# Kernel tuning notes

Measured on AMD Instinct MI355X. Metric: run time of the kernel, lower is better.

The kernel has to match this reference:

```python
import jax, jax.numpy as jnp
import numpy as np


def _hippo_scale_params(N, L):
    """Replicates HiPPOScale.__init__ for discretization='bilinear' (pure numpy)."""
    q = np.arange(N, dtype=np.float64)
    col, row = np.meshgrid(q, q)
    r = 2 * q + 1
    M = -(np.where(row >= col, r, 0) - np.diag(q))
    T = np.sqrt(np.diag(2 * q + 1))
    A = T @ M @ np.linalg.inv(T)          # (N, N)
    B = np.diag(T)                         # (N,)
    ts = np.arange(1, L + 1, dtype=np.float64)[:, None, None]  # (L,1,1)
    At = A[None] / ts                      # A / t, batched over t
    I = np.eye(N, dtype=np.float64)
    Mm = I[None] - 0.5 * At
    Nn = I[None] + 0.5 * At
    A_stacked = np.linalg.solve(Mm, Nn)                      # (L, N, N)
    Bt = B[None, :] / ts[:, 0, :]                             # (L, N)
    B_stacked = np.linalg.solve(Mm, Bt[..., None])[..., 0]    # (L, N)
    return A_stacked.astype(np.float32), B_stacked.astype(np.float32)


def setup_inputs() -> dict:
    N, L, Bsz = 64, 4096, 64
    key = jax.random.key(0)
    A_st, B_st = _hippo_scale_params(N, L)
    inputs = jax.random.normal(key, (L, Bsz), dtype=jnp.float32)
    return {
        "inputs": inputs,                       # (L, B)
        "A_stacked": jnp.asarray(A_st),         # (L, N, N)
        "B_stacked": jnp.asarray(B_st),         # (L, N)
    }


def reference(inputs, A_stacked, B_stacked):
    # u[t, b, :] = inputs[t, b] * B_stacked[t, :]   -> (L, B, N)
    u = inputs[..., None] * B_stacked[:, None, :]

    # x[t] = A[t] @ x[t-1] + u[t], x[-1] = 0  (time-varying linear recurrence).
    # The torch code computes this via a divide-and-conquer unroll; here we use
    # the equivalent parallel associative scan with elements (A, u) and
    # composition (A2@A1, A2@u1 + u2).
    def combine(e1, e2):
        a1, u1 = e1
        a2, u2 = e2
        a = jnp.matmul(a2, a1)                                  # (l, N, N)
        v = jnp.einsum('...ij,...bj->...bi', a2, u1) + u2       # (l, B, N)
        return (a, v)

    _, x = jax.lax.associative_scan(combine, (A_stacked, u))
    return x  # (L, B, N)
```

## Files before the change

kernel.cpp:

```cpp
#include <hip/hip_runtime.h>
#include <hip/hip_bf16.h>

#define TL 4096
#define NB 64
#define CH 8
#define CN 512
#define AS 72

typedef __attribute__((ext_vector_type(8))) short short8;
typedef __attribute__((ext_vector_type(4))) short short4v;
typedef __attribute__((ext_vector_type(4))) float floatx4;
typedef __attribute__((ext_vector_type(4))) unsigned int uint4v;

__device__ inline floatx4 mfma_bf16(short8 a, short8 b, floatx4 c) {
    return __builtin_amdgcn_mfma_f32_16x16x32_bf16(a, b, c, 0, 0, 0);
}

__device__ inline short bf16_rne(float x) {
    union { __hip_bfloat16 b; unsigned short s; } u;
    u.b = __float2bfloat16(x);
    return (short)u.s;
}

__device__ inline void split_bf16(float x, short& h, short& l) {
    h = bf16_rne(x);
    union { unsigned u; float f; } hv; hv.u = ((unsigned)(unsigned short)h) << 16;
    l = bf16_rne(x - hv.f);
}

__global__ __launch_bounds__(256, 2)
void hippo_phase1(const float* __restrict__ inp, const float* __restrict__ Ag,
                  const float* __restrict__ Bst,
                  unsigned* __restrict__ P32, float* __restrict__ VT)
{
    __shared__ short Ah[NB][AS], Al[NB][AS];
    __shared__ short SBh[NB][AS], SBl[NB][AS];
    __shared__ short VBh[NB][AS], VBl[NB][AS];

    const int tid = threadIdx.x;
    const int c = blockIdx.x, t0 = c * CH;
    const int w = tid >> 6, lane = tid & 63;
    const int quad = lane >> 4, l15 = lane & 15;
    const int wm = w >> 1, wb = w & 1;
    const int mr0 = 32*wm, br0 = 32*wb;

    floatx4 accS[2][2], accV[2][2];

    {
        const float* A0 = Ag + (size_t)t0 * 4096;
#pragma unroll
        for (int mi = 0; mi < 2; ++mi) {
            const int r0 = mr0 + 16*mi + 4*quad;
            float bt[4];
#pragma unroll
            for (int r = 0; r < 4; ++r) bt[r] = Bst[(size_t)t0*64 + r0 + r];
#pragma unroll
            for (int ni = 0; ni < 2; ++ni) {
                const int cc = br0 + 16*ni + l15;
                const float ii = inp[(size_t)t0*64 + cc];
#pragma unroll
                for (int r = 0; r < 4; ++r) {
                    accS[mi][ni][r] = A0[(size_t)(r0 + r)*64 + cc];
                    accV[mi][ni][r] = bt[r] * ii;
                }
            }
        }
    }

    float4 pre[4];
    float preB[2][4], preI[2];
    {
        const float4* Ap = (const float4*)(Ag + (size_t)(t0+1) * 4096);
#pragma unroll
        for (int q = 0; q < 4; ++q) pre[q] = Ap[tid + q*256];
#pragma unroll
        for (int mi = 0; mi < 2; ++mi)
#pragma unroll
            for (int r = 0; r < 4; ++r)
                preB[mi][r] = Bst[(size_t)(t0+1)*64 + mr0 + 16*mi + 4*quad + r];
        preI[0] = inp[(size_t)(t0+1)*64 + br0 + l15];
        preI[1] = inp[(size_t)(t0+1)*64 + br0 + 16 + l15];
    }

#pragma unroll
    for (int mi = 0; mi < 2; ++mi)
#pragma unroll
    for (int ni = 0; ni < 2; ++ni) {
        const int cc = br0 + 16*ni + l15, r0 = mr0 + 16*mi + 4*quad;
        short4v h4, l4;
#pragma unroll
        for (int r = 0; r < 4; ++r) { short hh,ll; split_bf16(accS[mi][ni][r],hh,ll); h4[r]=hh; l4[r]=ll; }
        *(short4v*)&SBh[cc][r0] = h4; *(short4v*)&SBl[cc][r0] = l4;
#pragma unroll
        for (int r = 0; r < 4; ++r) { short hh,ll; split_bf16(accV[mi][ni][r],hh,ll); h4[r]=hh; l4[r]=ll; }
        *(short4v*)&VBh[cc][r0] = h4; *(short4v*)&VBl[cc][r0] = l4;
    }

    for (int s = 1; s < CH; ++s) {
#pragma unroll
        for (int q = 0; q < 4; ++q) {
            int f = tid + q*256;
            int m = f >> 4, k0 = (f & 15)*4;
            float vv[4] = {pre[q].x, pre[q].y, pre[q].z, pre[q].w};
            short4v h4, l4;
#pragma unroll
            for (int r = 0; r < 4; ++r) { short hh,ll; split_bf16(vv[r],hh,ll); h4[r]=hh; l4[r]=ll; }
            *(short4v*)&Ah[m][k0] = h4; *(short4v*)&Al[m][k0] = l4;
        }
        float bcur[2][4], icur[2];
#pragma unroll
        for (int mi=0;mi<2;++mi)
#pragma unroll
            for (int r=0;r<4;++r) bcur[mi][r] = preB[mi][r];
        icur[0]=preI[0]; icur[1]=preI[1];
        if (s + 1 < CH) {
            const int t1 = t0 + s + 1;
            const float4* Ap = (const float4*)(Ag + (size_t)t1 * 4096);
#pragma unroll
            for (int q = 0; q < 4; ++q) pre[q] = Ap[tid + q*256];
#pragma unroll
            for (int mi=0;mi<2;++mi)
#pragma unroll
                for (int r=0;r<4;++r)
                    preB[mi][r] = Bst[(size_t)t1*64 + mr0 + 16*mi + 4*quad + r];
            preI[0] = inp[(size_t)t1*64 + br0 + l15];
            preI[1] = inp[(size_t)t1*64 + br0 + 16 + l15];
        }
        __syncthreads();

#pragma unroll
        for (int mi=0;mi<2;++mi)
#pragma unroll
        for (int ni=0;ni<2;++ni)
#pragma unroll
        for (int r=0;r<4;++r) {
            accS[mi][ni][r] = 0.0f;
            accV[mi][ni][r] = bcur[mi][r] * icur[ni];
        }
#pragma unroll
        for (int kc = 0; kc < 2; ++kc) {
            const int ko = 32*kc + 8*quad;
            short8 aH0 = *(const short8*)&Ah[mr0 + l15][ko];
            short8 aL0 = *(const short8*)&Al[mr0 + l15][ko];
            short8 aH1 = *(const short8*)&Ah[mr0 + 16 + l15][ko];
            short8 aL1 = *(const short8*)&Al[mr0 + 16 + l15][ko];
#pragma unroll
            for (int ni = 0; ni < 2; ++ni) {
                const int n = br0 + 16*ni + l15;
                short8 sH = *(const short8*)&SBh[n][ko];
                short8 sL = *(const short8*)&SBl[n][ko];
                short8 vH = *(const short8*)&VBh[n][ko];
                short8 vL = *(const short8*)&VBl[n][ko];
                accS[0][ni] = mfma_bf16(aH0, sH, accS[0][ni]);
                accS[0][ni] = mfma_bf16(aH0, sL, accS[0][ni]);
                accS[0][ni] = mfma_bf16(aL0, sH, accS[0][ni]);
                accS[1][ni] = mfma_bf16(aH1, sH, accS[1][ni]);
                accS[1][ni] = mfma_bf16(aH1, sL, accS[1][ni]);
                accS[1][ni] = mfma_bf16(aL1, sH, accS[1][ni]);
                accV[0][ni] = mfma_bf16(aH0, vH, accV[0][ni]);
                accV[0][ni] = mfma_bf16(aH0, vL, accV[0][ni]);
                accV[0][ni] = mfma_bf16(aL0, vH, accV[0][ni]);
                accV[1][ni] = mfma_bf16(aH1, vH, accV[1][ni]);
                accV[1][ni] = mfma_bf16(aH1, vL, accV[1][ni]);
                accV[1][ni] = mfma_bf16(aL1, vH, accV[1][ni]);
            }
        }
        __syncthreads();

        if (s + 1 < CH) {
#pragma unroll
            for (int mi = 0; mi < 2; ++mi)
#pragma unroll
            for (int ni = 0; ni < 2; ++ni) {
                const int cc = br0 + 16*ni + l15, r0 = mr0 + 16*mi + 4*quad;
                short4v h4, l4;
#pragma unroll
                for (int r = 0; r < 4; ++r) { short hh,ll; split_bf16(accS[mi][ni][r],hh,ll); h4[r]=hh; l4[r]=ll; }
                *(short4v*)&SBh[cc][r0] = h4; *(short4v*)&SBl[cc][r0] = l4;
#pragma unroll
                for (int r = 0; r < 4; ++r) { short hh,ll; split_bf16(accV[mi][ni][r],hh,ll); h4[r]=hh; l4[r]=ll; }
                *(short4v*)&VBh[cc][r0] = h4; *(short4v*)&VBl[cc][r0] = l4;
            }
        }
    }

    unsigned* po = P32 + (size_t)c * 4096;
#pragma unroll
    for (int mi = 0; mi < 2; ++mi)
#pragma unroll
    for (int ni = 0; ni < 2; ++ni) {
        const int cc = br0 + 16*ni + l15, r0 = mr0 + 16*mi + 4*quad;
        *(floatx4*)(VT + (size_t)c*4096 + cc*64 + r0) = accV[mi][ni];
#pragma unroll
        for (int r = 0; r < 4; ++r) {
            short hh, ll; split_bf16(accS[mi][ni][r], hh, ll);
            po[(r0 + r)*64 + cc] = ((unsigned)(unsigned short)hh << 16) | (unsigned)(unsigned short)ll;
        }
    }
}

__global__ __launch_bounds__(256, 2)
void hippo_seqscan(unsigned* __restrict__ P32, float* __restrict__ VT,
                   int bstride, int off0, int estride)
{
    __shared__ short PAh[NB][AS], PAl[NB][AS];
    __shared__ short PBh[NB][AS], PBl[NB][AS];
    __shared__ short VBh[NB][AS], VBl[NB][AS];

    const int tid = threadIdx.x;
    const int base = blockIdx.x * bstride + off0;
    const int w = tid >> 6, lane = tid & 63;
    const int quad = lane >> 4, l15 = lane & 15;
    const int wm = w >> 1, wb = w & 1;
    const int mr0 = 32*wm, br0 = 32*wb;

    {
        const unsigned* p0 = P32 + (size_t)base * 4096;
        const float*    v0 = VT  + (size_t)base * 4096;
#pragma unroll
        for (int q = 0; q < 4; ++q) {
            int f = tid + q * 256;
            int k = f & 63, m0 = (f >> 6) * 4;
            uint4v pk = *(const uint4v*)(p0 + k * 64 + m0);
#pragma unroll
            for (int r = 0; r < 4; ++r) {
                PBh[m0 + r][k] = (short)(pk[r] >> 16);
                PBl[m0 + r][k] = (short)(pk[r] & 0xFFFFu);
            }
        }
#pragma unroll
        for (int q = 0; q < 4; ++q) {
            int f = tid + q * 256;
            int n = f >> 4, k0 = (f & 15) * 4;
            float4 vv = *(const float4*)(v0 + n * 64 + k0);
            float va[4] = {vv.x, vv.y, vv.z, vv.w};
            short4v vh4, vl4;
#pragma unroll
            for (int r = 0; r < 4; ++r) { short hh, ll; split_bf16(va[r], hh, ll); vh4[r]=hh; vl4[r]=ll; }
            *(short4v*)&VBh[n][k0] = vh4; *(short4v*)&VBl[n][k0] = vl4;
        }
    }

    uint4v preA[4]; float4 preV[2][2];
    {
        const unsigned* pc = P32 + (size_t)(base + estride) * 4096;
        const float*    vc = VT  + (size_t)(base + estride) * 4096;
#pragma unroll
        for (int q = 0; q < 4; ++q) {
            int f = tid + q * 256;
            int m = f >> 4, k0 = (f & 15) * 4;
            preA[q] = *(const uint4v*)(pc + m * 64 + k0);
        }
#pragma unroll
        for (int mi = 0; mi < 2; ++mi)
#pragma unroll
        for (int ni = 0; ni < 2; ++ni) {
            const int cc = br0 + 16*ni + l15, r0 = mr0 + 16*mi + 4*quad;
            preV[mi][ni] = *(const float4*)(vc + cc * 64 + r0);
        }
    }

    for (int i = 1; i < 8; ++i) {
#pragma unroll
        for (int q = 0; q < 4; ++q) {
            int f = tid + q * 256;
            int m = f >> 4, k0 = (f & 15) * 4;
            short4v h4, l4;
#pragma unroll
            for (int r = 0; r < 4; ++r) { h4[r] = (short)(preA[q][r] >> 16); l4[r] = (short)(preA[q][r] & 0xFFFFu); }
            *(short4v*)&PAh[m][k0] = h4;
            *(short4v*)&PAl[m][k0] = l4;
        }
        floatx4 accP[2][2], accV[2][2];
#pragma unroll
        for (int mi = 0; mi < 2; ++mi)
#pragma unroll
        for (int ni = 0; ni < 2; ++ni) {
            accV[mi][ni][0] = preV[mi][ni].x; accV[mi][ni][1] = preV[mi][ni].y;
            accV[mi][ni][2] = preV[mi][ni].z; accV[mi][ni][3] = preV[mi][ni].w;
            accP[mi][ni][0]=accP[mi][ni][1]=accP[mi][ni][2]=accP[mi][ni][3]=0.0f;
        }
        if (i + 1 < 8) {
            const unsigned* pc = P32 + (size_t)(base + (i + 1) * estride) * 4096;
            const float*    vc = VT  + (size_t)(base + (i + 1) * estride) * 4096;
#pragma unroll
            for (int q = 0; q < 4; ++q) {
                int f = tid + q * 256;
                int m = f >> 4, k0 = (f & 15) * 4;
                preA[q] = *(const uint4v*)(pc + m * 64 + k0);
            }
#pragma unroll
            for (int mi = 0; mi < 2; ++mi)
#pragma unroll
            for (int ni = 0; ni < 2; ++ni) {
                const int cc = br0 + 16*ni + l15, r0 = mr0 + 16*mi + 4*quad;
                preV[mi][ni] = *(const float4*)(vc + cc * 64 + r0);
            }
        }
        __syncthreads();

#pragma unroll
        for (int kc = 0; kc < 2; ++kc) {
            const int ko = 32*kc + 8*quad;
            short8 aH0 = *(const short8*)&PAh[mr0 + l15][ko];
            short8 aL0 = *(const short8*)&PAl[mr0 + l15][ko];
            short8 aH1 = *(const short8*)&PAh[mr0 + 16 + l15][ko];
            short8 aL1 = *(const short8*)&PAl[mr0 + 16 + l15][ko];
#pragma unroll
            for (int ni = 0; ni < 2; ++ni) {
                const int n = br0 + 16*ni + l15;
                short8 pH = *(const short8*)&PBh[n][ko];
                short8 pL = *(const short8*)&PBl[n][ko];
                short8 vH = *(const short8*)&VBh[n][ko];
                short8 vL = *(const short8*)&VBl[n][ko];
                accP[0][ni] = mfma_bf16(aH0, pH, accP[0][ni]);
                accP[0][ni] = mfma_bf16(aH0, pL, accP[0][ni]);
                accP[0][ni] = mfma_bf16(aL0, pH, accP[0][ni]);
                accP[1][ni] = mfma_bf16(aH1, pH, accP[1][ni]);
                accP[1][ni] = mfma_bf16(aH1, pL, accP[1][ni]);
                accP[1][ni] = mfma_bf16(aL1, pH, accP[1][ni]);
                accV[0][ni] = mfma_bf16(aH0, vH, accV[0][ni]);
                accV[0][ni] = mfma_bf16(aH0, vL, accV[0][ni]);
                accV[0][ni] = mfma_bf16(aL0, vH, accV[0][ni]);
                accV[1][ni] = mfma_bf16(aH1, vH, accV[1][ni]);
                accV[1][ni] = mfma_bf16(aH1, vL, accV[1][ni]);
                accV[1][ni] = mfma_bf16(aL1, vH, accV[1][ni]);
            }
        }
        __syncthreads();

        const int idx = base + i * estride;
        unsigned* po = P32 + (size_t)idx * 4096;
#pragma unroll
        for (int mi = 0; mi < 2; ++mi)
#pragma unroll
        for (int ni = 0; ni < 2; ++ni) {
            const int cc = br0 + 16*ni + l15, r0 = mr0 + 16*mi + 4*quad;
            *(floatx4*)(VT + (size_t)idx * 4096 + cc * 64 + r0) = accV[mi][ni];
            short4v h4, l4;
#pragma unroll
            for (int r = 0; r < 4; ++r) {
                short hh, ll; split_bf16(accP[mi][ni][r], hh, ll);
                po[(r0 + r) * 64 + cc] = ((unsigned)(unsigned short)hh << 16) | (unsigned)(unsigned short)ll;
                h4[r] = hh; l4[r] = ll;
            }
            *(short4v*)&PBh[cc][r0] = h4; *(short4v*)&PBl[cc][r0] = l4;
#pragma unroll
            for (int r = 0; r < 4; ++r) { short hh,ll; split_bf16(accV[mi][ni][r],hh,ll); h4[r]=hh; l4[r]=ll; }
            *(short4v*)&VBh[cc][r0] = h4; *(short4v*)&VBl[cc][r0] = l4;
        }
    }
}

__global__ __launch_bounds__(256, 2)
void hippo_s3(unsigned* __restrict__ P32, const float* __restrict__ VT)
{
    __shared__ short PAh[NB][AS], PAl[NB][AS];
    __shared__ short EBh[NB][AS], EBl[NB][AS];
    const int tid = threadIdx.x;
    const int w = tid >> 6, lane = tid & 63, quad = lane >> 4, l15 = lane & 15;
    const int wm = w >> 1, wb = w & 1;
    const int mr0 = 32*wm, br0 = 32*wb;

#pragma unroll
    for (int q = 0; q < 16; ++q) {
        int f = tid + q * 256; EBh[f >> 6][f & 63] = 0; EBl[f >> 6][f & 63] = 0;
    }
    for (int s = 0; s < 7; ++s) {
        const int idx = 64 * s + 63;
        const unsigned* pc = P32 + (size_t)idx * 4096;
        const float*    vc = VT  + (size_t)idx * 4096;
#pragma unroll
        for (int q = 0; q < 4; ++q) {
            int f = tid + q * 256;
            int m = f >> 4, k0 = (f & 15) * 4;
            uint4v pk = *(const uint4v*)(pc + m * 64 + k0);
            short4v h4, l4;
#pragma unroll
            for (int r = 0; r < 4; ++r) { h4[r] = (short)(pk[r] >> 16); l4[r] = (short)(pk[r] & 0xFFFFu); }
            *(short4v*)&PAh[m][k0] = h4;
            *(short4v*)&PAl[m][k0] = l4;
        }
        floatx4 acc[2][2];
#pragma unroll
        for (int mi = 0; mi < 2; ++mi)
#pragma unroll
        for (int ni = 0; ni < 2; ++ni) {
            const int cc = br0 + 16*ni + l15, r0 = mr0 + 16*mi + 4*quad;
            float4 vv = *(const float4*)(vc + cc * 64 + r0);
            acc[mi][ni][0]=vv.x; acc[mi][ni][1]=vv.y; acc[mi][ni][2]=vv.z; acc[mi][ni][3]=vv.w;
        }
        __syncthreads();
#pragma unroll
        for (int kc = 0; kc < 2; ++kc) {
            const int ko = 32*kc + 8*quad;
            short8 aH0 = *(const short8*)&PAh[mr0 + l15][ko];
            short8 aL0 = *(const short8*)&PAl[mr0 + l15][ko];
            short8 aH1 = *(const short8*)&PAh[mr0 + 16 + l15][ko];
            short8 aL1 = *(const short8*)&PAl[mr0 + 16 + l15][ko];
#pragma unroll
            for (int ni = 0; ni < 2; ++ni) {
                const int n = br0 + 16*ni + l15;
                short8 eH = *(const short8*)&EBh[n][ko];
                short8 eL = *(const short8*)&EBl[n][ko];
                acc[0][ni] = mfma_bf16(aH0, eH, acc[0][ni]);
                acc[0][ni] = mfma_bf16(aH0, eL, acc[0][ni]);
                acc[0][ni] = mfma_bf16(aL0, eH, acc[0][ni]);
                acc[1][ni] = mfma_bf16(aH1, eH, acc[1][ni]);
                acc[1][ni] = mfma_bf16(aH1, eL, acc[1][ni]);
                acc[1][ni] = mfma_bf16(aL1, eH, acc[1][ni]);
            }
        }
        __syncthreads();
        float* eo = (float*)(P32 + (size_t)idx * 4096);
#pragma unroll
        for (int mi = 0; mi < 2; ++mi)
#pragma unroll
        for (int ni = 0; ni < 2; ++ni) {
            const int cc = br0 + 16*ni + l15, r0 = mr0 + 16*mi + 4*quad;
            *(floatx4*)(eo + cc * 64 + r0) = acc[mi][ni];
            short4v h4, l4;
#pragma unroll
            for (int r = 0; r < 4; ++r) { short hh,ll; split_bf16(acc[mi][ni][r],hh,ll); h4[r]=hh; l4[r]=ll; }
            *(short4v*)&EBh[cc][r0] = h4; *(short4v*)&EBl[cc][r0] = l4;
        }
    }
}

__global__ __launch_bounds__(256, 2)
void hippo_phase3(const float* __restrict__ inp, const float* __restrict__ Ag,
                  const float* __restrict__ Bst, const unsigned* __restrict__ P32,
                  const float* __restrict__ VT, float* __restrict__ out)
{
    __shared__ short Ah[NB][AS], Al[NB][AS];
    __shared__ short XBh[NB][AS], XBl[NB][AS];

    const int tid = threadIdx.x, c = blockIdx.x, t0 = c * CH;
    const int w = tid >> 6, lane = tid & 63, quad = lane >> 4, l15 = lane & 15;
    const int wm = w >> 1, wb = w & 1;
    const int mr0 = 32*wm, br0 = 32*wb;
    const int sup = c >> 6, g = c >> 3, gi = g & 7, j = c & 7;

    float4 pre[4];
    {
        const float4* Ap = (const float4*)(Ag + (size_t)t0 * 4096);
#pragma unroll
        for (int q = 0; q < 4; ++q) pre[q] = Ap[tid + q * 256];
    }

    if (sup == 0) {
#pragma unroll
        for (int q = 0; q < 16; ++q) { int f = tid + q*256; XBh[f>>6][f&63] = 0; XBl[f>>6][f&63] = 0; }
    } else {
        const float* e = (const float*)(P32 + (size_t)(64*(sup-1) + 63) * 4096);
#pragma unroll
        for (int q = 0; q < 4; ++q) {
            int f = tid + q*256; int b = f>>4, k0 = (f&15)*4;
            float4 v = *(const float4*)(e + b*64 + k0);
            float va[4] = {v.x,v.y,v.z,v.w};
            short4v h4, l4;
#pragma unroll
            for (int r=0;r<4;++r){short hh,ll;split_bf16(va[r],hh,ll);h4[r]=hh;l4[r]=ll;}
            *(short4v*)&XBh[b][k0] = h4; *(short4v*)&XBl[b][k0] = l4;
        }
    }

    auto combine = [&](int idx) {
        const unsigned* pc = P32 + (size_t)idx * 4096;
        const float*    vc = VT  + (size_t)idx * 4096;
#pragma unroll
        for (int q = 0; q < 4; ++q) {
            int f = tid + q*256;
            int m = f >> 4, k0 = (f & 15) * 4;
            uint4v pk = *(const uint4v*)(pc + m * 64 + k0);
            short4v h4, l4;
#pragma unroll
            for (int r = 0; r < 4; ++r) { h4[r] = (short)(pk[r] >> 16); l4[r] = (short)(pk[r] & 0xFFFFu); }
            *(short4v*)&Ah[m][k0] = h4;
            *(short4v*)&Al[m][k0] = l4;
        }
        floatx4 acc[2][2];
#pragma unroll
        for (int mi = 0; mi < 2; ++mi)
#pragma unroll
        for (int ni = 0; ni < 2; ++ni) {
            const int cc = br0 + 16*ni + l15, r0 = mr0 + 16*mi + 4*quad;
            float4 vv = *(const float4*)(vc + cc*64 + r0);
            acc[mi][ni][0]=vv.x; acc[mi][ni][1]=vv.y; acc[mi][ni][2]=vv.z; acc[mi][ni][3]=vv.w;
        }
        __syncthreads();
#pragma unroll
        for (int kc = 0; kc < 2; ++kc) {
            const int ko = 32*kc + 8*quad;
            short8 aH0 = *(const short8*)&Ah[mr0 + l15][ko];
            short8 aL0 = *(const short8*)&Al[mr0 + l15][ko];
            short8 aH1 = *(const short8*)&Ah[mr0 + 16 + l15][ko];
            short8 aL1 = *(const short8*)&Al[mr0 + 16 + l15][ko];
#pragma unroll
            for (int ni = 0; ni < 2; ++ni) {
                const int n = br0 + 16*ni + l15;
                short8 xH = *(const short8*)&XBh[n][ko];
                short8 xL = *(const short8*)&XBl[n][ko];
                acc[0][ni] = mfma_bf16(aH0, xH, acc[0][ni]);
                acc[0][ni] = mfma_bf16(aH0, xL, acc[0][ni]);
                acc[0][ni] = mfma_bf16(aL0, xH, acc[0][ni]);
                acc[1][ni] = mfma_bf16(aH1, xH, acc[1][ni]);
                acc[1][ni] = mfma_bf16(aH1, xL, acc[1][ni]);
                acc[1][ni] = mfma_bf16(aL1, xH, acc[1][ni]);
            }
        }
        __syncthreads();
#pragma unroll
        for (int mi = 0; mi < 2; ++mi)
#pragma unroll
        for (int ni = 0; ni < 2; ++ni) {
            const int cc = br0 + 16*ni + l15, r0 = mr0 + 16*mi + 4*quad;
            short4v h4, l4;
#pragma unroll
            for (int r=0;r<4;++r){short hh,ll;split_bf16(acc[mi][ni][r],hh,ll);h4[r]=hh;l4[r]=ll;}
            *(short4v*)&XBh[cc][r0] = h4; *(short4v*)&XBl[cc][r0] = l4;
        }
    };
    if (gi) combine(8*g - 1);
    if (j)  combine(c - 1);

    float preB[2][4], preI[2];
#pragma unroll
    for (int mi = 0; mi < 2; ++mi)
#pragma unroll
        for (int r = 0; r < 4; ++r)
            preB[mi][r] = Bst[(size_t)t0*64 + mr0 + 16*mi + 4*quad + r];
    preI[0] = inp[(size_t)t0*64 + br0 + l15];
    preI[1] = inp[(size_t)t0*64 + br0 + 16 + l15];

    floatx4 acc[2][2];
    for (int s = 0; s < CH; ++s) {
        const int t = t0 + s;
#pragma unroll
        for (int q = 0; q < 4; ++q) {
            int f = tid + q*256; int m = f>>4, k0 = (f&15)*4;
            float vv[4] = {pre[q].x,pre[q].y,pre[q].z,pre[q].w};
            short4v h4, l4;
#pragma unroll
            for (int r=0;r<4;++r){short hh,ll;split_bf16(vv[r],hh,ll);h4[r]=hh;l4[r]=ll;}
            *(short4v*)&Ah[m][k0] = h4; *(short4v*)&Al[m][k0] = l4;
        }
        float bcur[2][4], icur[2];
#pragma unroll
        for (int mi=0;mi<2;++mi)
#pragma unroll
            for (int r=0;r<4;++r) bcur[mi][r] = preB[mi][r];
        icur[0]=preI[0]; icur[1]=preI[1];
        if (s + 1 < CH) {
            const int t1 = t + 1;
            const float4* Ap = (const float4*)(Ag + (size_t)t1 * 4096);
#pragma unroll
            for (int q = 0; q < 4; ++q) pre[q] = Ap[tid + q * 256];
#pragma unroll
            for (int mi=0;mi<2;++mi)
#pragma unroll
                for (int r=0;r<4;++r)
                    preB[mi][r] = Bst[(size_t)t1*64 + mr0 + 16*mi + 4*quad + r];
            preI[0] = inp[(size_t)t1*64 + br0 + l15];
            preI[1] = inp[(size_t)t1*64 + br0 + 16 + l15];
        }
        __syncthreads();

#pragma unroll
        for (int mi=0;mi<2;++mi)
#pragma unroll
        for (int ni=0;ni<2;++ni)
#pragma unroll
        for (int r=0;r<4;++r) acc[mi][ni][r] = bcur[mi][r] * icur[ni];
#pragma unroll
        for (int kc = 0; kc < 2; ++kc) {
            const int ko = 32*kc + 8*quad;
            short8 aH0 = *(const short8*)&Ah[mr0 + l15][ko];
            short8 aL0 = *(const short8*)&Al[mr0 + l15][ko];
            short8 aH1 = *(const short8*)&Ah[mr0 + 16 + l15][ko];
            short8 aL1 = *(const short8*)&Al[mr0 + 16 + l15][ko];
#pragma unroll
            for (int ni = 0; ni < 2; ++ni) {
                const int n = br0 + 16*ni + l15;
                short8 xH = *(const short8*)&XBh[n][ko];
                short8 xL = *(const short8*)&XBl[n][ko];
                acc[0][ni] = mfma_bf16(aH0, xH, acc[0][ni]);
                acc[0][ni] = mfma_bf16(aH0, xL, acc[0][ni]);
                acc[0][ni] = mfma_bf16(aL0, xH, acc[0][ni]);
                acc[1][ni] = mfma_bf16(aH1, xH, acc[1][ni]);
                acc[1][ni] = mfma_bf16(aH1, xL, acc[1][ni]);
                acc[1][ni] = mfma_bf16(aL1, xH, acc[1][ni]);
            }
        }
        __syncthreads();
#pragma unroll
        for (int mi = 0; mi < 2; ++mi)
#pragma unroll
        for (int ni = 0; ni < 2; ++ni) {
            const int cc = br0 + 16*ni + l15, r0 = mr0 + 16*mi + 4*quad;
            *(floatx4*)(out + (size_t)t*4096 + cc*64 + r0) = acc[mi][ni];
            if (s + 1 < CH) {
                short4v h4, l4;
#pragma unroll
                for (int r=0;r<4;++r){short hh,ll;split_bf16(acc[mi][ni][r],hh,ll);h4[r]=hh;l4[r]=ll;}
                *(short4v*)&XBh[cc][r0] = h4; *(short4v*)&XBl[cc][r0] = l4;
            }
        }
    }
}

extern "C" void kernel_launch(void* const* d_in, const int* in_sizes, int n_in,
                              void* d_out, int out_size, void* d_ws, size_t ws_size,
                              hipStream_t stream)
{
    const float* inp = (const float*)d_in[0];
    const float* A   = (const float*)d_in[1];
    const float* Bst = (const float*)d_in[2];
    float* out = (float*)d_out;
    float* ws  = (float*)d_ws;

    unsigned* P32 = (unsigned*)ws;
    float*    VT  = ws + (size_t)CN * 4096;

    hippo_phase1<<<CN, 256, 0, stream>>>(inp, A, Bst, P32, VT);
    hippo_seqscan<<<64, 256, 0, stream>>>(P32, VT, 8, 0, 1);
    hippo_seqscan<<<8, 256, 0, stream>>>(P32, VT, 64, 7, 8);
    hippo_s3<<<1, 256, 0, stream>>>(P32, VT);
    hippo_phase3<<<CN, 256, 0, stream>>>(inp, A, Bst, P32, VT, out);
}
```

Baseline: 180.1 us.

## Load A fragments directly into registers and double-buffer LDS state tiles

Each wave now loads its own MFMA A-operand fragments from global memory straight into registers and splits them into bf16 hi/lo there, instead of staging the whole A matrix through shared memory. The state/value tiles in LDS are double-buffered, which removes one __syncthreads per step in all three kernels. This cuts LDS traffic and barrier stalls on the sequential chain. In exchange, register pressure rises and global loads become per-wave strided reads rather than fully coalesced block-wide float4 loads.

New measurement: 200.6 us. 1.11x slower.

```diff
diff --git a/kernel.cpp b/kernel.cpp
--- a/kernel.cpp
+++ b/kernel.cpp
@@ -15,17 +15,27 @@
 __device__ inline floatx4 mfma_bf16(short8 a, short8 b, floatx4 c) {
     return __builtin_amdgcn_mfma_f32_16x16x32_bf16(a, b, c, 0, 0, 0);
 }
-
 __device__ inline short bf16_rne(float x) {
     union { __hip_bfloat16 b; unsigned short s; } u;
     u.b = __float2bfloat16(x);
     return (short)u.s;
 }
-
 __device__ inline void split_bf16(float x, short& h, short& l) {
     h = bf16_rne(x);
     union { unsigned u; float f; } hv; hv.u = ((unsigned)(unsigned short)h) << 16;
     l = bf16_rne(x - hv.f);
+}
+__device__ inline void cvt_frag(float4 a, float4 b, short8& H, short8& L) {
+    float v[8] = {a.x,a.y,a.z,a.w,b.x,b.y,b.z,b.w};
+#pragma unroll
+    for (int r = 0; r < 8; ++r) { short hh,ll; split_bf16(v[r],hh,ll); H[r]=hh; L[r]=ll; }
+}
+__device__ inline void unpack_frag(uint4v a, uint4v b, short8& H, short8& L) {
+#pragma unroll
+    for (int r = 0; r < 4; ++r) {
+        H[r]   = (short)(a[r] >> 16); L[r]   = (short)(a[r] & 0xFFFFu);
+        H[4+r] = (short)(b[r] >> 16); L[4+r] = (short)(b[r] & 0xFFFFu);
+    }
 }
 
 __global__ __launch_bounds__(256, 2)
@@ -33,9 +43,8 @@
                   const float* __restrict__ Bst,
                   unsigned* __restrict__ P32, float* __restrict__ VT)
 {
-    __shared__ short Ah[NB][AS], Al[NB][AS];
-    __shared__ short SBh[NB][AS], SBl[NB][AS];
-    __shared__ short VBh[NB][AS], VBl[NB][AS];
+    __shared__ short SBh[2][NB][AS], SBl[2][NB][AS];
+    __shared__ short VBh[2][NB][AS], VBl[2][NB][AS];
 
     const int tid = threadIdx.x;
     const int c = blockIdx.x, t0 = c * CH;
@@ -43,145 +52,149 @@
     const int quad = lane >> 4, l15 = lane & 15;
     const int wm = w >> 1, wb = w & 1;
     const int mr0 = 32*wm, br0 = 32*wb;
+    const int row0 = mr0 + l15;
+    const int wr0  = mr0 + 4*quad;
+    const int col0 = br0 + l15;
+
+    float4 rA[2][2][2];
+#pragma unroll
+    for (int mi = 0; mi < 2; ++mi)
+#pragma unroll
+    for (int kc = 0; kc < 2; ++kc) {
+        const float* p = Ag + (size_t)(t0+1)*4096 + (row0 + 16*mi)*64 + 32*kc + 8*quad;
+        rA[mi][kc][0] = *(const float4*)p;
+        rA[mi][kc][1] = *(const float4*)(p + 4);
+    }
+    float4 bcur[2], bnxt[2]; float icur[2], inxt[2];
+#pragma unroll
+    for (int mi = 0; mi < 2; ++mi) {
+        bcur[mi] = *(const float4*)(Bst + (size_t)t0*64 + wr0 + 16*mi);
+        bnxt[mi] = *(const float4*)(Bst + (size_t)(t0+1)*64 + wr0 + 16*mi);
+    }
+    icur[0] = inp[(size_t)t0*64 + col0];
+    icur[1] = inp[(size_t)t0*64 + col0 + 16];
+    inxt[0] = inp[(size_t)(t0+1)*64 + col0];
+    inxt[1] = inp[(size_t)(t0+1)*64 + col0 + 16];
 
     floatx4 accS[2][2], accV[2][2];
-
     {
         const float* A0 = Ag + (size_t)t0 * 4096;
-#pragma unroll
-        for (int mi = 0; mi < 2; ++mi) {
-            const int r0 = mr0 + 16*mi + 4*quad;
-            float bt[4];
-#pragma unroll
-            for (int r = 0; r < 4; ++r) bt[r] = Bst[(size_t)t0*64 + r0 + r];
-#pragma unroll
-            for (int ni = 0; ni < 2; ++ni) {
-                const int cc = br0 + 16*ni + l15;
-                const float ii = inp[(size_t)t0*64 + cc];
-#pragma unroll
-                for (int r = 0; r < 4; ++r) {
-                    accS[mi][ni][r] = A0[(size_t)(r0 + r)*64 + cc];
-                    accV[mi][ni][r] = bt[r] * ii;
-                }
-            }
-        }
-    }
-
-    float4 pre[4];
-    float preB[2][4], preI[2];
-    {
-        const float4* Ap = (const float4*)(Ag + (size_t)(t0+1) * 4096);
-#pragma unroll
-        for (int q = 0; q < 4; ++q) pre[q] = Ap[tid + q*256];
-#pragma unroll
-        for (int mi = 0; mi < 2; ++mi)
-#pragma unroll
-            for (int r = 0; r < 4; ++r)
-                preB[mi][r] = Bst[(size_t)(t0+1)*64 + mr0 + 16*mi + 4*quad + r];
-        preI[0] = inp[(size_t)(t0+1)*64 + br0 + l15];
-        preI[1] = inp[(size_t)(t0+1)*64 + br0 + 16 + l15];
-    }
+        float bc[2][4] = {{bcur[0].x,bcur[0].y,bcur[0].z,bcur[0].w},
+                          {bcur[1].x,bcur[1].y,bcur[1].z,bcur[1].w}};
+#pragma unroll
+        for (int mi = 0; mi < 2; ++mi)
+#pragma unroll
+        for (int ni = 0; ni < 2; ++ni) {
+#pragma unroll
+            for (int r = 0; r < 4; ++r) {
+                accS[mi][ni][r] = A0[(size_t)(wr0 + 16*mi + r)*64 + col0 + 16*ni];
+                accV[mi][ni][r] = bc[mi][r] * icur[ni];
+            }
+        }
+    }
+    short8 aH[2][2], aL[2][2];
+#pragma unroll
+    for (int mi = 0; mi < 2; ++mi)
+#pragma unroll
+    for (int kc = 0; kc < 2; ++kc)
+        cvt_frag(rA[mi][kc][0], rA[mi][kc][1], aH[mi][kc], aL[mi][kc]);
 
 #pragma unroll
     for (int mi = 0; mi < 2; ++mi)
 #pragma unroll
     for (int ni = 0; ni < 2; ++ni) {
-        const int cc = br0 + 16*ni + l15, r0 = mr0 + 16*mi + 4*quad;
+        const int cc = col0 + 16*ni, r0 = wr0 + 16*mi;
         short4v h4, l4;
 #pragma unroll
         for (int r = 0; r < 4; ++r) { short hh,ll; split_bf16(accS[mi][ni][r],hh,ll); h4[r]=hh; l4[r]=ll; }
-        *(short4v*)&SBh[cc][r0] = h4; *(short4v*)&SBl[cc][r0] = l4;
+        *(short4v*)&SBh[0][cc][r0] = h4; *(short4v*)&SBl[0][cc][r0] = l4;
 #pragma unroll
         for (int r = 0; r < 4; ++r) { short hh,ll; split_bf16(accV[mi][ni][r],hh,ll); h4[r]=hh; l4[r]=ll; }
-        *(short4v*)&VBh[cc][r0] = h4; *(short4v*)&VBl[cc][r0] = l4;
-    }
+        *(short4v*)&VBh[0][cc][r0] = h4; *(short4v*)&VBl[0][cc][r0] = l4;
+    }
+    __syncthreads();
+
+    int cur = 0;
+    bcur[0]=bnxt[0]; bcur[1]=bnxt[1]; icur[0]=inxt[0]; icur[1]=inxt[1];
 
     for (int s = 1; s < CH; ++s) {
-#pragma unroll
-        for (int q = 0; q < 4; ++q) {
-            int f = tid + q*256;
-            int m = f >> 4, k0 = (f & 15)*4;
-            float vv[4] = {pre[q].x, pre[q].y, pre[q].z, pre[q].w};
-            short4v h4, l4;
-#pragma unroll
-            for (int r = 0; r < 4; ++r) { short hh,ll; split_bf16(vv[r],hh,ll); h4[r]=hh; l4[r]=ll; }
-            *(short4v*)&Ah[m][k0] = h4; *(short4v*)&Al[m][k0] = l4;
-        }
-        float bcur[2][4], icur[2];
-#pragma unroll
-        for (int mi=0;mi<2;++mi)
-#pragma unroll
-            for (int r=0;r<4;++r) bcur[mi][r] = preB[mi][r];
-        icur[0]=preI[0]; icur[1]=preI[1];
         if (s + 1 < CH) {
             const int t1 = t0 + s + 1;
-            const float4* Ap = (const float4*)(Ag + (size_t)t1 * 4096);
-#pragma unroll
-            for (int q = 0; q < 4; ++q) pre[q] = Ap[tid + q*256];
-#pragma unroll
-            for (int mi=0;mi<2;++mi)
-#pragma unroll
-                for (int r=0;r<4;++r)
-                    preB[mi][r] = Bst[(size_t)t1*64 + mr0 + 16*mi + 4*quad + r];
-            preI[0] = inp[(size_t)t1*64 + br0 + l15];
-            preI[1] = inp[(size_t)t1*64 + br0 + 16 + l15];
-        }
-        __syncthreads();
-
-#pragma unroll
-        for (int mi=0;mi<2;++mi)
-#pragma unroll
-        for (int ni=0;ni<2;++ni)
-#pragma unroll
-        for (int r=0;r<4;++r) {
-            accS[mi][ni][r] = 0.0f;
-            accV[mi][ni][r] = bcur[mi][r] * icur[ni];
+#pragma unroll
+            for (int mi = 0; mi < 2; ++mi)
+#pragma unroll
+            for (int kc = 0; kc < 2; ++kc) {
+                const float* p = Ag + (size_t)t1*4096 + (row0 + 16*mi)*64 + 32*kc + 8*quad;
+                rA[mi][kc][0] = *(const float4*)p;
+                rA[mi][kc][1] = *(const float4*)(p + 4);
+            }
+#pragma unroll
+            for (int mi = 0; mi < 2; ++mi)
+                bnxt[mi] = *(const float4*)(Bst + (size_t)t1*64 + wr0 + 16*mi);
+            inxt[0] = inp[(size_t)t1*64 + col0];
+            inxt[1] = inp[(size_t)t1*64 + col0 + 16];
+        }
+        {
+            float bc[2][4] = {{bcur[0].x,bcur[0].y,bcur[0].z,bcur[0].w},
+                              {bcur[1].x,bcur[1].y,bcur[1].z,bcur[1].w}};
+#pragma unroll
+            for (int mi = 0; mi < 2; ++mi)
+#pragma unroll
+            for (int ni = 0; ni < 2; ++ni)
+#pragma unroll
+            for (int r = 0; r < 4; ++r) {
+                accS[mi][ni][r] = 0.0f;
+                accV[mi][ni][r] = bc[mi][r] * icur[ni];
+            }
         }
 #pragma unroll
         for (int kc = 0; kc < 2; ++kc) {
             const int ko = 32*kc + 8*quad;
-            short8 aH0 = *(const short8*)&Ah[mr0 + l15][ko];
-            short8 aL0 = *(const short8*)&Al[mr0 + l15][ko];
-            short8 aH1 = *(const short8*)&Ah[mr0 + 16 + l15][ko];
-            short8 aL1 = *(const short8*)&Al[mr0 + 16 + l15][ko];
 #pragma unroll
             for (int ni = 0; ni < 2; ++ni) {
-                const int n = br0 + 16*ni + l15;
-                short8 sH = *(const short8*)&SBh[n][ko];
-                short8 sL = *(const short8*)&SBl[n][ko];
-                short8 vH = *(const short8*)&VBh[n][ko];
-                short8 vL = *(const short8*)&VBl[n][ko];
-                accS[0][ni] = mfma_bf16(aH0, sH, accS[0][ni]);
-                accS[0][ni] = mfma_bf16(aH0, sL, accS[0][ni]);
-                accS[0][ni] = mfma_bf16(aL0, sH, accS[0][ni]);
-                accS[1][ni] = mfma_bf16(aH1, sH, accS[1][ni]);
-                accS[1][ni] = mfma_bf16(aH1, sL, accS[1][ni]);
-                accS[1][ni] = mfma_bf16(aL1, sH, accS[1][ni]);
-                accV[0][ni] = mfma_bf16(aH0, vH, accV[0][ni]);
-                accV[0][ni] = mfma_bf16(aH0, vL, accV[0][ni]);
-                accV[0][ni] = mfma_bf16(aL0, vH, accV[0][ni]);
-                accV[1][ni] = mfma_bf16(aH1, vH, accV[1][ni]);
-                accV[1][ni] = mfma_bf16(aH1, vL, accV[1][ni]);
-                accV[1][ni] = mfma_bf16(aL1, vH, accV[1][ni]);
-            }
-        }
-        __syncthreads();
-
+                const int n = col0 + 16*ni;
+                short8 sH = *(const short8*)&SBh[cur][n][ko];
+                short8 sL = *(const short8*)&SBl[cur][n][ko];
+                short8 vH = *(const short8*)&VBh[cur][n][ko];
+                short8 vL = *(const short8*)&VBl[cur][n][ko];
+                accS[0][ni] = mfma_bf16(aH[0][kc], sH, accS[0][ni]);
+                accS[0][ni] = mfma_bf16(aH[0][kc], sL, accS[0][ni]);
+                accS[0][ni] = mfma_bf16(aL[0][kc], sH, accS[0][ni]);
+                accS[1][ni] = mfma_bf16(aH[1][kc], sH, accS[1][ni]);
+                accS[1][ni] = mfma_bf16(aH[1][kc], sL, accS[1][ni]);
+                accS[1][ni] = mfma_bf16(aL[1][kc], sH, accS[1][ni]);
+                accV[0][ni] = mfma_bf16(aH[0][kc], vH, accV[0][ni]);
+                accV[0][ni] = mfma_bf16(aH[0][kc], vL, accV[0][ni]);
+                accV[0][ni] = mfma_bf16(aL[0][kc], vH, accV[0][ni]);
+                accV[1][ni] = mfma_bf16(aH[1][kc], vH, accV[1][ni]);
+                accV[1][ni] = mfma_bf16(aH[1][kc], vL, accV[1][ni]);
+                accV[1][ni] = mfma_bf16(aL[1][kc], vH, accV[1][ni]);
+            }
+        }
         if (s + 1 < CH) {
 #pragma unroll
             for (int mi = 0; mi < 2; ++mi)
 #pragma unroll
+            for (int kc = 0; kc < 2; ++kc)
+                cvt_frag(rA[mi][kc][0], rA[mi][kc][1], aH[mi][kc], aL[mi][kc]);
+            const int nb = cur ^ 1;
+#pragma unroll
+            for (int mi = 0; mi < 2; ++mi)
+#pragma unroll
             for (int ni = 0; ni < 2; ++ni) {
-                const int cc = br0 + 16*ni + l15, r0 = mr0 + 16*mi + 4*quad;
+                const int cc = col0 + 16*ni, r0 = wr0 + 16*mi;
                 short4v h4, l4;
 #pragma unroll
                 for (int r = 0; r < 4; ++r) { short hh,ll; split_bf16(accS[mi][ni][r],hh,ll); h4[r]=hh; l4[r]=ll; }
-                *(short4v*)&SBh[cc][r0] = h4; *(short4v*)&SBl[cc][r0] = l4;
+                *(short4v*)&SBh[nb][cc][r0] = h4; *(short4v*)&SBl[nb][cc][r0] = l4;
 #pragma unroll
                 for (int r = 0; r < 4; ++r) { short hh,ll; split_bf16(accV[mi][ni][r],hh,ll); h4[r]=hh; l4[r]=ll; }
-                *(short4v*)&VBh[cc][r0] = h4; *(short4v*)&VBl[cc][r0] = l4;
-            }
-        }
+                *(short4v*)&VBh[nb][cc][r0] = h4; *(short4v*)&VBl[nb][cc][r0] = l4;
+            }
+            __syncthreads();
+        }
+        cur ^= 1;
+        bcur[0]=bnxt[0]; bcur[1]=bnxt[1]; icur[0]=inxt[0]; icur[1]=inxt[1];
     }
 
     unsigned* po = P32 + (size_t)c * 4096;
@@ -189,12 +202,12 @@
     for (int mi = 0; mi < 2; ++mi)
 #pragma unroll
     for (int ni = 0; ni < 2; ++ni) {
-        const int cc = br0 + 16*ni + l15, r0 = mr0 + 16*mi + 4*quad;
+        const int cc = col0 + 16*ni, r0 = wr0 + 16*mi;
         *(floatx4*)(VT + (size_t)c*4096 + cc*64 + r0) = accV[mi][ni];
 #pragma unroll
         for (int r = 0; r < 4; ++r) {
             short hh, ll; split_bf16(accS[mi][ni][r], hh, ll);
-            po[(r0 + r)*64 + cc] = ((unsigned)(unsigned short)hh << 16) | (unsigned)(unsigned short)ll;
+            po[(size_t)(r0 + r)*64 + cc] = ((unsigned)(unsigned short)hh << 16) | (unsigned)(unsigned short)ll;
         }
     }
 }
@@ -203,9 +216,8 @@
 void hippo_seqscan(unsigned* __restrict__ P32, float* __restrict__ VT,
                    int bstride, int off0, int estride)
 {
-    __shared__ short PAh[NB][AS], PAl[NB][AS];
-    __shared__ short PBh[NB][AS], PBl[NB][AS];
-    __shared__ short VBh[NB][AS], VBl[NB][AS];
+    __shared__ short PBh[2][NB][AS], PBl[2][NB][AS];
+    __shared__ short VBh[2][NB][AS], VBl[2][NB][AS];
 
     const int tid = threadIdx.x;
     const int base = blockIdx.x * bstride + off0;
@@ -213,6 +225,9 @@
     const int quad = lane >> 4, l15 = lane & 15;
     const int wm = w >> 1, wb = w & 1;
     const int mr0 = 32*wm, br0 = 32*wb;
+    const int row0 = mr0 + l15;
+    const int wr0  = mr0 + 4*quad;
+    const int col0 = br0 + l15;
 
     {
         const unsigned* p0 = P32 + (size_t)base * 4096;
@@ -224,8 +239,8 @@
             uint4v pk = *(const uint4v*)(p0 + k * 64 + m0);
 #pragma unroll
             for (int r = 0; r < 4; ++r) {
-                PBh[m0 + r][k] = (short)(pk[r] >> 16);
-                PBl[m0 + r][k] = (short)(pk[r] & 0xFFFFu);
+                PBh[0][m0 + r][k] = (short)(pk[r] >> 16);
+                PBl[0][m0 + r][k] = (short)(pk[r] & 0xFFFFu);
             }
         }
 #pragma unroll
@@ -237,40 +252,39 @@
             short4v vh4, vl4;
 #pragma unroll
             for (int r = 0; r < 4; ++r) { short hh, ll; split_bf16(va[r], hh, ll); vh4[r]=hh; vl4[r]=ll; }
-            *(short4v*)&VBh[n][k0] = vh4; *(short4v*)&VBl[n][k0] = vl4;
-        }
-    }
-
-    uint4v preA[4]; float4 preV[2][2];
+            *(short4v*)&VBh[0][n][k0] = vh4; *(short4v*)&VBl[0][n][k0] = vl4;
+        }
+    }
+    uint4v rP[2][2][2]; float4 preV[2][2];
     {
         const unsigned* pc = P32 + (size_t)(base + estride) * 4096;
         const float*    vc = VT  + (size_t)(base + estride) * 4096;
 #pragma unroll
-        for (int q = 0; q < 4; ++q) {
-            int f = tid + q * 256;
-            int m = f >> 4, k0 = (f & 15) * 4;
-            preA[q] = *(const uint4v*)(pc + m * 64 + k0);
-        }
-#pragma unroll
-        for (int mi = 0; mi < 2; ++mi)
-#pragma unroll
-        for (int ni = 0; ni < 2; ++ni) {
-            const int cc = br0 + 16*ni + l15, r0 = mr0 + 16*mi + 4*quad;
-            preV[mi][ni] = *(const float4*)(vc + cc * 64 + r0);
-        }
-    }
-
+        for (int mi = 0; mi < 2; ++mi)
+#pragma unroll
+        for (int kc = 0; kc < 2; ++kc) {
+            const unsigned* p = pc + (size_t)(row0 + 16*mi)*64 + 32*kc + 8*quad;
+            rP[mi][kc][0] = *(const uint4v*)p;
+            rP[mi][kc][1] = *(const uint4v*)(p + 4);
+        }
+#pragma unroll
+        for (int mi = 0; mi < 2; ++mi)
+#pragma unroll
+        for (int ni = 0; ni < 2; ++ni)
+            preV[mi][ni] = *(const float4*)(vc + (size_t)(col0 + 16*ni)*64 + wr0 + 16*mi);
+    }
+    __syncthreads();
+
+    short8 aH[2][2], aL[2][2];
+#pragma unroll
+    for (int mi = 0; mi < 2; ++mi)
+#pragma unroll
+    for (int kc = 0; kc < 2; ++kc)
+        unpack_frag(rP[mi][kc][0], rP[mi][kc][1], aH[mi][kc], aL[mi][kc]);
+
+    int cur = 0;
     for (int i = 1; i < 8; ++i) {
-#pragma unroll
-        for (int q = 0; q < 4; ++q) {
-            int f = tid + q * 256;
-            int m = f >> 4, k0 = (f & 15) * 4;
-            short4v h4, l4;
-#pragma unroll
-            for (int r = 0; r < 4; ++r) { h4[r] = (short)(preA[q][r] >> 16); l4[r] = (short)(preA[q][r] & 0xFFFFu); }
-            *(short4v*)&PAh[m][k0] = h4;
-            *(short4v*)&PAl[m][k0] = l4;
-        }
+        const int idx = base + i * estride;
         floatx4 accP[2][2], accV[2][2];
 #pragma unroll
         for (int mi = 0; mi < 2; ++mi)
@@ -281,149 +295,193 @@
             accP[mi][ni][0]=accP[mi][ni][1]=accP[mi][ni][2]=accP[mi][ni][3]=0.0f;
         }
         if (i + 1 < 8) {
-            const unsigned* pc = P32 + (size_t)(base + (i + 1) * estride) * 4096;
-            const float*    vc = VT  + (size_t)(base + (i + 1) * estride) * 4096;
-#pragma unroll
-            for (int q = 0; q < 4; ++q) {
-                int f = tid + q * 256;
-                int m = f >> 4, k0 = (f & 15) * 4;
-                preA[q] = *(const uint4v*)(pc + m * 64 + k0);
-            }
-#pragma unroll
-            for (int mi = 0; mi < 2; ++mi)
+            const unsigned* pc = P32 + (size_t)(base + (i+1) * estride) * 4096;
+            const float*    vc = VT  + (size_t)(base + (i+1) * estride) * 4096;
+#pragma unroll
+            for (int mi = 0; mi < 2; ++mi)
+#pragma unroll
+            for (int kc = 0; kc < 2; ++kc) {
+                const unsigned* p = pc + (size_t)(row0 + 16*mi)*64 + 32*kc + 8*quad;
+                rP[mi][kc][0] = *(const uint4v*)p;
+                rP[mi][kc][1] = *(const uint4v*)(p + 4);
+            }
+#pragma unroll
+            for (int mi = 0; mi < 2; ++mi)
+#pragma unroll
+            for (int ni = 0; ni < 2; ++ni)
+                preV[mi][ni] = *(const float4*)(vc + (size_t)(col0 + 16*ni)*64 + wr0 + 16*mi);
+        }
+#pragma unroll
+        for (int kc = 0; kc < 2; ++kc) {
+            const int ko = 32*kc + 8*quad;
 #pragma unroll
             for (int ni = 0; ni < 2; ++ni) {
-                const int cc = br0 + 16*ni + l15, r0 = mr0 + 16*mi + 4*quad;
-                preV[mi][ni] = *(const float4*)(vc + cc * 64 + r0);
-            }
-        }
-        __syncthreads();
-
-#pragma unroll
-        for (int kc = 0; kc < 2; ++kc) {
-            const int ko = 32*kc + 8*quad;
-            short8 aH0 = *(const short8*)&PAh[mr0 + l15][ko];
-            short8 aL0 = *(const short8*)&PAl[mr0 + l15][ko];
-            short8 aH1 = *(const short8*)&PAh[mr0 + 16 + l15][ko];
-            short8 aL1 = *(const short8*)&PAl[mr0 + 16 + l15][ko];
-#pragma unroll
-            for (int ni = 0; ni < 2; ++ni) {
-                const int n = br0 + 16*ni + l15;
-                short8 pH = *(const short8*)&PBh[n][ko];
-                short8 pL = *(const short8*)&PBl[n][ko];
-                short8 vH = *(const short8*)&VBh[n][ko];
-                short8 vL = *(const short8*)&VBl[n][ko];
-                accP[0][ni] = mfma_bf16(aH0, pH, accP[0][ni]);
-                accP[0][ni] = mfma_bf16(aH0, pL, accP[0][ni]);
-                accP[0][ni] = mfma_bf16(aL0, pH, accP[0][ni]);
-                accP[1][ni] = mfma_bf16(aH1, pH, accP[1][ni]);
-                accP[1][ni] = mfma_bf16(aH1, pL, accP[1][ni]);
-                accP[1][ni] = mfma_bf16(aL1, pH, accP[1][ni]);
-                accV[0][ni] = mfma_bf16(aH0, vH, accV[0][ni]);
-                accV[0][ni] = mfma_bf16(aH0, vL, accV[0][ni]);
-                accV[0][ni] = mfma_bf16(aL0, vH, accV[0][ni]);
-                accV[1][ni] = mfma_bf16(aH1, vH, accV[1][ni]);
-                accV[1][ni] = mfma_bf16(aH1, vL, accV[1][ni]);
-                accV[1][ni] = mfma_bf16(aL1, vH, accV[1][ni]);
-            }
-        }
-        __syncthreads();
-
-        const int idx = base + i * estride;
+                const int n = col0 + 16*ni;
+                short8 pH = *(const short8*)&PBh[cur][n][ko];
+                short8 pL = *(const short8*)&PBl[cur][n][ko];
+                short8 vH = *(const short8*)&VBh[cur][n][ko];
+                short8 vL = *(const short8*)&VBl[cur][n][ko];
+                accP[0][ni] = mfma_bf16(aH[0][kc], pH, accP[0][ni]);
+                accP[0][ni] = mfma_bf16(aH[0][kc], pL, accP[0][ni]);
+                accP[0][ni] = mfma_bf16(aL[0][kc], pH, accP[0][ni]);
+                accP[1][ni] = mfma_bf16(aH[1][kc], pH, accP[1][ni]);
+                accP[1][ni] = mfma_bf16(aH[1][kc], pL, accP[1][ni]);
+                accP[1][ni] = mfma_bf16(aL[1][kc], pH, accP[1][ni]);
+                accV[0][ni] = mfma_bf16(aH[0][kc], vH, accV[0][ni]);
+                accV[0][ni] = mfma_bf16(aH[0][kc], vL, accV[0][ni]);
+                accV[0][ni] = mfma_bf16(aL[0][kc], vH, accV[0][ni]);
+                accV[1][ni] = mfma_bf16(aH[1][kc], vH, accV[1][ni]);
+                accV[1][ni] = mfma_bf16(aH[1][kc], vL, accV[1][ni]);
+                accV[1][ni] = mfma_bf16(aL[1][kc], vH, accV[1][ni]);
+            }
+        }
+        if (i + 1 < 8) {
+#pragma unroll
+            for (int mi = 0; mi < 2; ++mi)
+#pragma unroll
+            for (int kc = 0; kc < 2; ++kc)
+                unpack_frag(rP[mi][kc][0], rP[mi][kc][1], aH[mi][kc], aL[mi][kc]);
+        }
         unsigned* po = P32 + (size_t)idx * 4096;
-#pragma unroll
-        for (int mi = 0; mi < 2; ++mi)
-#pragma unroll
-        for (int ni = 0; ni < 2; ++ni) {
-            const int cc = br0 + 16*ni + l15, r0 = mr0 + 16*mi + 4*quad;
-            *(floatx4*)(VT + (size_t)idx * 4096 + cc * 64 + r0) = accV[mi][ni];
+        const int nb = cur ^ 1;
+#pragma unroll
+        for (int mi = 0; mi < 2; ++mi)
+#pragma unroll
+        for (int ni = 0; ni < 2; ++ni) {
+            const int cc = col0 + 16*ni, r0 = wr0 + 16*mi;
+            *(floatx4*)(VT + (size_t)idx*4096 + cc*64 + r0) = accV[mi][ni];
             short4v h4, l4;
 #pragma unroll
             for (int r = 0; r < 4; ++r) {
                 short hh, ll; split_bf16(accP[mi][ni][r], hh, ll);
-                po[(r0 + r) * 64 + cc] = ((unsigned)(unsigned short)hh << 16) | (unsigned)(unsigned short)ll;
-                h4[r] = hh; l4[r] = ll;
-            }
-            *(short4v*)&PBh[cc][r0] = h4; *(short4v*)&PBl[cc][r0] = l4;
-#pragma unroll
-            for (int r = 0; r < 4; ++r) { short hh,ll; split_bf16(accV[mi][ni][r],hh,ll); h4[r]=hh; l4[r]=ll; }
-            *(short4v*)&VBh[cc][r0] = h4; *(short4v*)&VBl[cc][r0] = l4;
-        }
+                po[(size_t)(r0+r)*64 + cc] = ((unsigned)(unsigned short)hh << 16) | (unsigned)(unsigned short)ll;
+                h4[r]=hh; l4[r]=ll;
+            }
+            if (i + 1 < 8) {
+                *(short4v*)&PBh[nb][cc][r0] = h4; *(short4v*)&PBl[nb][cc][r0] = l4;
+                short4v vh4, vl4;
+#pragma unroll
+                for (int r = 0; r < 4; ++r) { short hh,ll; split_bf16(accV[mi][ni][r],hh,ll); vh4[r]=hh; vl4[r]=ll; }
+                *(short4v*)&VBh[nb][cc][r0] = vh4; *(short4v*)&VBl[nb][cc][r0] = vl4;
+            }
+        }
+        if (i + 1 < 8) __syncthreads();
+        cur ^= 1;
     }
 }
 
 __global__ __launch_bounds__(256, 2)
 void hippo_s3(unsigned* __restrict__ P32, const float* __restrict__ VT)
 {
-    __shared__ short PAh[NB][AS], PAl[NB][AS];
-    __shared__ short EBh[NB][AS], EBl[NB][AS];
+    __shared__ short EBh[2][NB][AS], EBl[2][NB][AS];
     const int tid = threadIdx.x;
     const int w = tid >> 6, lane = tid & 63, quad = lane >> 4, l15 = lane & 15;
     const int wm = w >> 1, wb = w & 1;
     const int mr0 = 32*wm, br0 = 32*wb;
+    const int row0 = mr0 + l15;
+    const int wr0  = mr0 + 4*quad;
+    const int col0 = br0 + l15;
 
 #pragma unroll
     for (int q = 0; q < 16; ++q) {
-        int f = tid + q * 256; EBh[f >> 6][f & 63] = 0; EBl[f >> 6][f & 63] = 0;
-    }
+        int f = tid + q * 256; EBh[0][f >> 6][f & 63] = 0; EBl[0][f >> 6][f & 63] = 0;
+    }
+    uint4v rP[2][2][2]; float4 preV[2][2];
+    {
+        const unsigned* pc = P32 + (size_t)63 * 4096;
+        const float*    vc = VT  + (size_t)63 * 4096;
+#pragma unroll
+        for (int mi = 0; mi < 2; ++mi)
+#pragma unroll
+        for (int kc = 0; kc < 2; ++kc) {
+            const unsigned* p = pc + (size_t)(row0 + 16*mi)*64 + 32*kc + 8*quad;
+            rP[mi][kc][0] = *(const uint4v*)p;
+            rP[mi][kc][1] = *(const uint4v*)(p + 4);
+        }
+#pragma unroll
+        for (int mi = 0; mi < 2; ++mi)
+#pragma unroll
+        for (int ni = 0; ni < 2; ++ni)
+            preV[mi][ni] = *(const float4*)(vc + (size_t)(col0 + 16*ni)*64 + wr0 + 16*mi);
+    }
+    __syncthreads();
+
+    short8 aH[2][2], aL[2][2];
+#pragma unroll
+    for (int mi = 0; mi < 2; ++mi)
+#pragma unroll
+    for (int kc = 0; kc < 2; ++kc)
+        unpack_frag(rP[mi][kc][0], rP[mi][kc][1], aH[mi][kc], aL[mi][kc]);
+
+    int cur = 0;
     for (int s = 0; s < 7; ++s) {
         const int idx = 64 * s + 63;
-        const unsigned* pc = P32 + (size_t)idx * 4096;
-        const float*    vc = VT  + (size_t)idx * 4096;
-#pragma unroll
-        for (int q = 0; q < 4; ++q) {
-            int f = tid + q * 256;
-            int m = f >> 4, k0 = (f & 15) * 4;
-            uint4v pk = *(const uint4v*)(pc + m * 64 + k0);
-            short4v h4, l4;
-#pragma unroll
-            for (int r = 0; r < 4; ++r) { h4[r] = (short)(pk[r] >> 16); l4[r] = (short)(pk[r] & 0xFFFFu); }
-            *(short4v*)&PAh[m][k0] = h4;
-            *(short4v*)&PAl[m][k0] = l4;
-        }
         floatx4 acc[2][2];
 #pragma unroll
         for (int mi = 0; mi < 2; ++mi)
 #pragma unroll
         for (int ni = 0; ni < 2; ++ni) {
-            const int cc = br0 + 16*ni + l15, r0 = mr0 + 16*mi + 4*quad;
-            float4 vv = *(const float4*)(vc + cc * 64 + r0);
-            acc[mi][ni][0]=vv.x; acc[mi][ni][1]=vv.y; acc[mi][ni][2]=vv.z; acc[mi][ni][3]=vv.w;
-        }
-        __syncthreads();
+            acc[mi][ni][0] = preV[mi][ni].x; acc[mi][ni][1] = preV[mi][ni].y;
+            acc[mi][ni][2] = preV[mi][ni].z; acc[mi][ni][3] = preV[mi][ni].w;
+        }
+        if (s + 1 < 7) {
+            const int idx2 = 64 * (s + 1) + 63;
+            const unsigned* pc = P32 + (size_t)idx2 * 4096;
+            const float*    vc = VT  + (size_t)idx2 * 4096;
+#pragma unroll
+            for (int mi = 0; mi < 2; ++mi)
+#pragma unroll
+            for (int kc = 0; kc < 2; ++kc) {
+                const unsigned* p = pc + (size_t)(row0 + 16*mi)*64 + 32*kc + 8*quad;
+                rP[mi][kc][0] = *(const uint4v*)p;
+                rP[mi][kc][1] = *(const uint4v*)(p + 4);
+            }
+#pragma unroll
+            for (int mi = 0; mi < 2; ++mi)
+#pragma unroll
+            for (int ni = 0; ni < 2; ++ni)
+                preV[mi][ni] = *(const float4*)(vc + (size_t)(col0 + 16*ni)*64 + wr0 + 16*mi);
+        }
 #pragma unroll
         for (int kc = 0; kc < 2; ++kc) {
             const int ko = 32*kc + 8*quad;
-            short8 aH0 = *(const short8*)&PAh[mr0 + l15][ko];
-            short8 aL0 = *(const short8*)&PAl[mr0 + l15][ko];
-            short8 aH1 = *(const short8*)&PAh[mr0 + 16 + l15][ko];
-            short8 aL1 = *(const short8*)&PAl[mr0 + 16 + l15][ko];
 #pragma unroll
             for (int ni = 0; ni < 2; ++ni) {
-                const int n = br0 + 16*ni + l15;
-                short8 eH = *(const short8*)&EBh[n][ko];
-                short8 eL = *(const short8*)&EBl[n][ko];
-                acc[0][ni] = mfma_bf16(aH0, eH, acc[0][ni]);
-                acc[0][ni] = mfma_bf16(aH0, eL, acc[0][ni]);
-                acc[0][ni] = mfma_bf16(aL0, eH, acc[0][ni]);
-                acc[1][ni] = mfma_bf16(aH1, eH, acc[1][ni]);
-                acc[1][ni] = mfma_bf16(aH1, eL, acc[1][ni]);
-                acc[1][ni] = mfma_bf16(aL1, eH, acc[1][ni]);
-            }
-        }
-        __syncthreads();
+                const int n = col0 + 16*ni;
+                short8 eH = *(const short8*)&EBh[cur][n][ko];
+                short8 eL = *(const short8*)&EBl[cur][n][ko];
+                acc[0][ni] = mfma_bf16(aH[0][kc], eH, acc[0][ni]);
+                acc[0][ni] = mfma_bf16(aH[0][kc], eL, acc[0][ni]);
+                acc[0][ni] = mfma_bf16(aL[0][kc], eH, acc[0][ni]);
+                acc[1][ni] = mfma_bf16(aH[1][kc], eH, acc[1][ni]);
+                acc[1][ni] = mfma_bf16(aH[1][kc], eL, acc[1][ni]);
+                acc[1][ni] = mfma_bf16(aL[1][kc], eH, acc[1][ni]);
+            }
+        }
+        if (s + 1 < 7) {
+#pragma unroll
+            for (int mi = 0; mi < 2; ++mi)
+#pragma unroll
+            for (int kc = 0; kc < 2; ++kc)
+                unpack_frag(rP[mi][kc][0], rP[mi][kc][1], aH[mi][kc], aL[mi][kc]);
+        }
         float* eo = (float*)(P32 + (size_t)idx * 4096);
-#pragma unroll
-        for (int mi = 0; mi < 2; ++mi)
-#pragma unroll
-        for (int ni = 0; ni < 2; ++ni) {
-            const int cc = br0 + 16*ni + l15, r0 = mr0 + 16*mi + 4*quad;
-            *(floatx4*)(eo + cc * 64 + r0) = acc[mi][ni];
-            short4v h4, l4;
-#pragma unroll
-            for (int r = 0; r < 4; ++r) { short hh,ll; split_bf16(acc[mi][ni][r],hh,ll); h4[r]=hh; l4[r]=ll; }
-            *(short4v*)&EBh[cc][r0] = h4; *(short4v*)&EBl[cc][r0] = l4;
-        }
+        const int nb = cur ^ 1;
+#pragma unroll
+        for (int mi = 0; mi < 2; ++mi)
+#pragma unroll
+        for (int ni = 0; ni < 2; ++ni) {
+            const int cc = col0 + 16*ni, r0 = wr0 + 16*mi;
+            *(floatx4*)(eo + cc*64 + r0) = acc[mi][ni];
+            if (s + 1 < 7) {
+                short4v h4, l4;
+#pragma unroll
+                for (int r = 0; r < 4; ++r) { short hh,ll; split_bf16(acc[mi][ni][r],hh,ll); h4[r]=hh; l4[r]=ll; }
+                *(short4v*)&EBh[nb][cc][r0] = h4; *(short4v*)&EBl[nb][cc][r0] = l4;
+            }
+        }
+        if (s + 1 < 7) __syncthreads();
+        cur ^= 1;
     }
 }
 
@@ -432,25 +490,36 @@
                   const float* __restrict__ Bst, const unsigned* __restrict__ P32,
                   const float* __restrict__ VT, float* __restrict__ out)
 {
-    __shared__ short Ah[NB][AS], Al[NB][AS];
-    __shared__ short XBh[NB][AS], XBl[NB][AS];
+    __shared__ short XBh[2][NB][AS], XBl[2][NB][AS];
 
     const int tid = threadIdx.x, c = blockIdx.x, t0 = c * CH;
     const int w = tid >> 6, lane = tid & 63, quad = lane >> 4, l15 = lane & 15;
     const int wm = w >> 1, wb = w & 1;
     const int mr0 = 32*wm, br0 = 32*wb;
+    const int row0 = mr0 + l15;
+    const int wr0  = mr0 + 4*quad;
+    const int col0 = br0 + l15;
     const int sup = c >> 6, g = c >> 3, gi = g & 7, j = c & 7;
 
-    float4 pre[4];
-    {
-        const float4* Ap = (const float4*)(Ag + (size_t)t0 * 4096);
-#pragma unroll
-        for (int q = 0; q < 4; ++q) pre[q] = Ap[tid + q * 256];
-    }
+    float4 rA[2][2][2];
+#pragma unroll
+    for (int mi = 0; mi < 2; ++mi)
+#pragma unroll
+    for (int kc = 0; kc < 2; ++kc) {
+        const float* p = Ag + (size_t)t0*4096 + (row0 + 16*mi)*64 + 32*kc + 8*quad;
+        rA[mi][kc][0] = *(const float4*)p;
+        rA[mi][kc][1] = *(const float4*)(p + 4);
+    }
+    float4 bcur[2], bnxt[2]; float icur[2], inxt[2];
+#pragma unroll
+    for (int mi = 0; mi < 2; ++mi)
+        bcur[mi] = *(const float4*)(Bst + (size_t)t0*64 + wr0 + 16*mi);
+    icur[0] = inp[(size_t)t0*64 + col0];
+    icur[1] = inp[(size_t)t0*64 + col0 + 16];
 
     if (sup == 0) {
 #pragma unroll
-        for (int q = 0; q < 16; ++q) { int f = tid + q*256; XBh[f>>6][f&63] = 0; XBl[f>>6][f&63] = 0; }
+        for (int q = 0; q < 16; ++q) { int f = tid + q*256; XBh[0][f>>6][f&63] = 0; XBl[0][f>>6][f&63] = 0; }
     } else {
         const float* e = (const float*)(P32 + (size_t)(64*(sup-1) + 63) * 4096);
 #pragma unroll
@@ -461,151 +530,147 @@
             short4v h4, l4;
 #pragma unroll
             for (int r=0;r<4;++r){short hh,ll;split_bf16(va[r],hh,ll);h4[r]=hh;l4[r]=ll;}
-            *(short4v*)&XBh[b][k0] = h4; *(short4v*)&XBl[b][k0] = l4;
-        }
-    }
+            *(short4v*)&XBh[0][b][k0] = h4; *(short4v*)&XBl[0][b][k0] = l4;
+        }
+    }
+    __syncthreads();
+    int cur = 0;
 
     auto combine = [&](int idx) {
+        uint4v rP[2][2][2];
         const unsigned* pc = P32 + (size_t)idx * 4096;
         const float*    vc = VT  + (size_t)idx * 4096;
 #pragma unroll
-        for (int q = 0; q < 4; ++q) {
-            int f = tid + q*256;
-            int m = f >> 4, k0 = (f & 15) * 4;
-            uint4v pk = *(const uint4v*)(pc + m * 64 + k0);
+        for (int mi = 0; mi < 2; ++mi)
+#pragma unroll
+        for (int kc = 0; kc < 2; ++kc) {
+            const unsigned* p = pc + (size_t)(row0 + 16*mi)*64 + 32*kc + 8*quad;
+            rP[mi][kc][0] = *(const uint4v*)p;
+            rP[mi][kc][1] = *(const uint4v*)(p + 4);
+        }
+        floatx4 acc[2][2];
+#pragma unroll
+        for (int mi = 0; mi < 2; ++mi)
+#pragma unroll
+        for (int ni = 0; ni < 2; ++ni) {
+            float4 vv = *(const float4*)(vc + (size_t)(col0 + 16*ni)*64 + wr0 + 16*mi);
+            acc[mi][ni][0]=vv.x; acc[mi][ni][1]=vv.y; acc[mi][ni][2]=vv.z; acc[mi][ni][3]=vv.w;
+        }
+        short8 cH[2][2], cL[2][2];
+#pragma unroll
+        for (int mi = 0; mi < 2; ++mi)
+#pragma unroll
+        for (int kc = 0; kc < 2; ++kc)
+            unpack_frag(rP[mi][kc][0], rP[mi][kc][1], cH[mi][kc], cL[mi][kc]);
+#pragma unroll
+        for (int kc = 0; kc < 2; ++kc) {
+            const int ko = 32*kc + 8*quad;
+#pragma unroll
+            for (int ni = 0; ni < 2; ++ni) {
+                const int n = col0 + 16*ni;
+                short8 xH = *(const short8*)&XBh[cur][n][ko];
+                short8 xL = *(const short8*)&XBl[cur][n][ko];
+                acc[0][ni] = mfma_bf16(cH[0][kc], xH, acc[0][ni]);
+                acc[0][ni] = mfma_bf16(cH[0][kc], xL, acc[0][ni]);
+                acc[0][ni] = mfma_bf16(cL[0][kc], xH, acc[0][ni]);
+                acc[1][ni] = mfma_bf16(cH[1][kc], xH, acc[1][ni]);
+                acc[1][ni] = mfma_bf16(cH[1][kc], xL, acc[1][ni]);
+                acc[1][ni] = mfma_bf16(cL[1][kc], xH, acc[1][ni]);
+            }
+        }
+        const int nb = cur ^ 1;
+#pragma unroll
+        for (int mi = 0; mi < 2; ++mi)
+#pragma unroll
+        for (int ni = 0; ni < 2; ++ni) {
+            const int cc = col0 + 16*ni, r0 = wr0 + 16*mi;
             short4v h4, l4;
 #pragma unroll
-            for (int r = 0; r < 4; ++r) { h4[r] = (short)(pk[r] >> 16); l4[r] = (short)(pk[r] & 0xFFFFu); }
-            *(short4v*)&Ah[m][k0] = h4;
-            *(short4v*)&Al[m][k0] = l4;
-        }
-        floatx4 acc[2][2];
-#pragma unroll
-        for (int mi = 0; mi < 2; ++mi)
-#pragma unroll
-        for (int ni = 0; ni < 2; ++ni) {
-            const int cc = br0 + 16*ni + l15, r0 = mr0 + 16*mi + 4*quad;
-            float4 vv = *(const float4*)(vc + cc*64 + r0);
-            acc[mi][ni][0]=vv.x; acc[mi][ni][1]=vv.y; acc[mi][ni][2]=vv.z; acc[mi][ni][3]=vv.w;
+            for (int r=0;r<4;++r){short hh,ll;split_bf16(acc[mi][ni][r],hh,ll);h4[r]=hh;l4[r]=ll;}
+            *(short4v*)&XBh[nb][cc][r0] = h4; *(short4v*)&XBl[nb][cc][r0] = l4;
         }
         __syncthreads();
-#pragma unroll
-        for (int kc = 0; kc < 2; ++kc) {
-            const int ko = 32*kc + 8*quad;
-            short8 aH0 = *(const short8*)&Ah[mr0 + l15][ko];
-            short8 aL0 = *(const short8*)&Al[mr0 + l15][ko];
-            short8 aH1 = *(const short8*)&Ah[mr0 + 16 + l15][ko];
-            short8 aL1 = *(const short8*)&Al[mr0 + 16 + l15][ko];
-#pragma unroll
-            for (int ni = 0; ni < 2; ++ni) {
-                const int n = br0 + 16*ni + l15;
-                short8 xH = *(const short8*)&XBh[n][ko];
-                short8 xL = *(const short8*)&XBl[n][ko];
-                acc[0][ni] = mfma_bf16(aH0, xH, acc[0][ni]);
-                acc[0][ni] = mfma_bf16(aH0, xL, acc[0][ni]);
-                acc[0][ni] = mfma_bf16(aL0, xH, acc[0][ni]);
-                acc[1][ni] = mfma_bf16(aH1, xH, acc[1][ni]);
-                acc[1][ni] = mfma_bf16(aH1, xL, acc[1][ni]);
-                acc[1][ni] = mfma_bf16(aL1, xH, acc[1][ni]);
-            }
-        }
-        __syncthreads();
-#pragma unroll
-        for (int mi = 0; mi < 2; ++mi)
-#pragma unroll
-        for (int ni = 0; ni < 2; ++ni) {
-            const int cc = br0 + 16*ni + l15, r0 = mr0 + 16*mi + 4*quad;
-            short4v h4, l4;
-#pragma unroll
-            for (int r=0;r<4;++r){short hh,ll;split_bf16(acc[mi][ni][r],hh,ll);h4[r]=hh;l4[r]=ll;}
-            *(short4v*)&XBh[cc][r0] = h4; *(short4v*)&XBl[cc][r0] = l4;
-        }
+        cur ^= 1;
     };
     if (gi) combine(8*g - 1);
     if (j)  combine(c - 1);
 
-    float preB[2][4], preI[2];
-#pragma unroll
-    for (int mi = 0; mi < 2; ++mi)
-#pragma unroll
-        for (int r = 0; r < 4; ++r)
-            preB[mi][r] = Bst[(size_t)t0*64 + mr0 + 16*mi + 4*quad + r];
-    preI[0] = inp[(size_t)t0*64 + br0 + l15];
-    preI[1] = inp[(size_t)t0*64 + br0 + 16 + l15];
+    short8 aH[2][2], aL[2][2];
+#pragma unroll
+    for (int mi = 0; mi < 2; ++mi)
+#pragma unroll
+    for (int kc = 0; kc < 2; ++kc)
+        cvt_frag(rA[mi][kc][0], rA[mi][kc][1], aH[mi][kc], aL[mi][kc]);
 
     floatx4 acc[2][2];
     for (int s = 0; s < CH; ++s) {
         const int t = t0 + s;
-#pragma unroll
-        for (int q = 0; q < 4; ++q) {
-            int f = tid + q*256; int m = f>>4, k0 = (f&15)*4;
-            float vv[4] = {pre[q].x,pre[q].y,pre[q].z,pre[q].w};
-            short4v h4, l4;
-#pragma unroll
-            for (int r=0;r<4;++r){short hh,ll;split_bf16(vv[r],hh,ll);h4[r]=hh;l4[r]=ll;}
-            *(short4v*)&Ah[m][k0] = h4; *(short4v*)&Al[m][k0] = l4;
-        }
-        float bcur[2][4], icur[2];
-#pragma unroll
-        for (int mi=0;mi<2;++mi)
-#pragma unroll
-            for (int r=0;r<4;++r) bcur[mi][r] = preB[mi][r];
-        icur[0]=preI[0]; icur[1]=preI[1];
         if (s + 1 < CH) {
             const int t1 = t + 1;
-            const float4* Ap = (const float4*)(Ag + (size_t)t1 * 4096);
-#pragma unroll
-            for (int q = 0; q < 4; ++q) pre[q] = Ap[tid + q * 256];
+#pragma unroll
+            for (int mi = 0; mi < 2; ++mi)
+#pragma unroll
+            for (int kc = 0; kc < 2; ++kc) {
+                const float* p = Ag + (size_t)t1*4096 + (row0 + 16*mi)*64 + 32*kc + 8*quad;
+                rA[mi][kc][0] = *(const float4*)p;
+                rA[mi][kc][1] = *(const float4*)(p + 4);
+            }
+#pragma unroll
+            for (int mi = 0; mi < 2; ++mi)
+                bnxt[mi] = *(const float4*)(Bst + (size_t)t1*64 + wr0 + 16*mi);
+            inxt[0] = inp[(size_t)t1*64 + col0];
+            inxt[1] = inp[(size_t)t1*64 + col0 + 16];
+        }
+        {
+            float bc[2][4] = {{bcur[0].x,bcur[0].y,bcur[0].z,bcur[0].w},
+                              {bcur[1].x,bcur[1].y,bcur[1].z,bcur[1].w}};
 #pragma unroll
             for (int mi=0;mi<2;++mi)
 #pragma unroll
-                for (int r=0;r<4;++r)
-                    preB[mi][r] = Bst[(size_t)t1*64 + mr0 + 16*mi + 4*quad + r];
-            preI[0] = inp[(size_t)t1*64 + br0 + l15];
-            preI[1] = inp[(size_t)t1*64 + br0 + 16 + l15];
-        }
-        __syncthreads();
-
-#pragma unroll
-        for (int mi=0;mi<2;++mi)
-#pragma unroll
-        for (int ni=0;ni<2;++ni)
-#pragma unroll
-        for (int r=0;r<4;++r) acc[mi][ni][r] = bcur[mi][r] * icur[ni];
+            for (int ni=0;ni<2;++ni)
+#pragma unroll
+            for (int r=0;r<4;++r) acc[mi][ni][r] = bc[mi][r] * icur[ni];
+        }
 #pragma unroll
         for (int kc = 0; kc < 2; ++kc) {
             const int ko = 32*kc + 8*quad;
-            short8 aH0 = *(const short8*)&Ah[mr0 + l15][ko];
-            short8 aL0 = *(const short8*)&Al[mr0 + l15][ko];
-            short8 aH1 = *(const short8*)&Ah[mr0 + 16 + l15][ko];
-            short8 aL1 = *(const short8*)&Al[mr0 + 16 + l15][ko];
 #pragma unroll
             for (int ni = 0; ni < 2; ++ni) {
-                const int n = br0 + 16*ni + l15;
-                short8 xH = *(const short8*)&XBh[n][ko];
-                short8 xL = *(const short8*)&XBl[n][ko];
-                acc[0][ni] = mfma_bf16(aH0, xH, acc[0][ni]);
-                acc[0][ni] = mfma_bf16(aH0, xL, acc[0][ni]);
-                acc[0][ni] = mfma_bf16(aL0, xH, acc[0][ni]);
-                acc[1][ni] = mfma_bf16(aH1, xH, acc[1][ni]);
-                acc[1][ni] = mfma_bf16(aH1, xL, acc[1][ni]);
-                acc[1][ni] = mfma_bf16(aL1, xH, acc[1][ni]);
-            }
-        }
-        __syncthreads();
-#pragma unroll
-        for (int mi = 0; mi < 2; ++mi)
-#pragma unroll
-        for (int ni = 0; ni < 2; ++ni) {
-            const int cc = br0 + 16*ni + l15, r0 = mr0 + 16*mi + 4*quad;
+                const int n = col0 + 16*ni;
+                short8 xH = *(const short8*)&XBh[cur][n][ko];
+                short8 xL = *(const short8*)&XBl[cur][n][ko];
+                acc[0][ni] = mfma_bf16(aH[0][kc], xH, acc[0][ni]);
+                acc[0][ni] = mfma_bf16(aH[0][kc], xL, acc[0][ni]);
+                acc[0][ni] = mfma_bf16(aL[0][kc], xH, acc[0][ni]);
+                acc[1][ni] = mfma_bf16(aH[1][kc], xH, acc[1][ni]);
+                acc[1][ni] = mfma_bf16(aH[1][kc], xL, acc[1][ni]);
+                acc[1][ni] = mfma_bf16(aL[1][kc], xH, acc[1][ni]);
+            }
+        }
+        if (s + 1 < CH) {
+#pragma unroll
+            for (int mi = 0; mi < 2; ++mi)
+#pragma unroll
+            for (int kc = 0; kc < 2; ++kc)
+                cvt_frag(rA[mi][kc][0], rA[mi][kc][1], aH[mi][kc], aL[mi][kc]);
+        }
+        const int nb = cur ^ 1;
+#pragma unroll
+        for (int mi = 0; mi < 2; ++mi)
+#pragma unroll
+        for (int ni = 0; ni < 2; ++ni) {
+            const int cc = col0 + 16*ni, r0 = wr0 + 16*mi;
             *(floatx4*)(out + (size_t)t*4096 + cc*64 + r0) = acc[mi][ni];
             if (s + 1 < CH) {
                 short4v h4, l4;
 #pragma unroll
                 for (int r=0;r<4;++r){short hh,ll;split_bf16(acc[mi][ni][r],hh,ll);h4[r]=hh;l4[r]=ll;}
-                *(short4v*)&XBh[cc][r0] = h4; *(short4v*)&XBl[cc][r0] = l4;
-            }
-        }
+                *(short4v*)&XBh[nb][cc][r0] = h4; *(short4v*)&XBl[nb][cc][r0] = l4;
+            }
+        }
+        if (s + 1 < CH) __syncthreads();
+        cur ^= 1;
+        bcur[0]=bnxt[0]; bcur[1]=bnxt[1]; icur[0]=inxt[0]; icur[1]=inxt[1];
     }
 }
 
```
